# Kernel tuning notes

Hardware: AMD Instinct MI355X
Metric: run time of the kernel (lower is better)

The kernel has to match this reference:

```python
import jax, jax.numpy as jnp
import numpy as np

N_NODES = 100000
N_EDGES = 3200000
IN_DIM = 128
H1, F1 = 8, 8          # layer1: 8 heads x 8 feats -> concat 64
N_CLASSES = 40         # layer2: 1 head -> classes
NEG_SLOPE = 0.2        # GAT LeakyReLU slope


def setup_inputs() -> dict:
    key = jax.random.key(0)
    ks = jax.random.split(key, 8)
    x = jax.random.normal(ks[0], (N_NODES, IN_DIM), dtype=jnp.float32)
    adj = jax.random.randint(ks[1], (2, N_EDGES), 0, N_NODES, dtype=jnp.int64)
    s1 = 1.0 / np.sqrt(IN_DIM)
    s2 = 1.0 / np.sqrt(H1 * F1)
    W1 = jax.random.normal(ks[2], (IN_DIM, H1 * F1), dtype=jnp.float32) * s1
    a1_src = jax.random.normal(ks[3], (H1, F1), dtype=jnp.float32) * s2
    a1_dst = jax.random.normal(ks[4], (H1, F1), dtype=jnp.float32) * s2
    W2 = jax.random.normal(ks[5], (H1 * F1, N_CLASSES), dtype=jnp.float32) * s2
    a2_src = jax.random.normal(ks[6], (1, N_CLASSES), dtype=jnp.float32) * s2
    a2_dst = jax.random.normal(ks[7], (1, N_CLASSES), dtype=jnp.float32) * s2
    return {"input_matrix": x, "adjacency_coo_matrix": adj,
            "W1": W1, "a1_src": a1_src, "a1_dst": a1_dst,
            "W2": W2, "a2_src": a2_src, "a2_dst": a2_dst}


def gat_layer(x, src, dst, W, a_s, a_d, heads, fdim):
    n = x.shape[0]
    h = (x @ W).reshape(n, heads, fdim)                 # [N,H,F]
    e_src = jnp.sum(h * a_s, axis=-1)                   # [N,H]
    e_dst = jnp.sum(h * a_d, axis=-1)                   # [N,H]
    e = jax.nn.leaky_relu(e_src[src] + e_dst[dst], NEG_SLOPE)  # [E,H]
    m = jax.ops.segment_max(e, dst, num_segments=n)     # per-dst softmax max
    p = jnp.exp(e - m[dst])
    s = jax.ops.segment_sum(p, dst, num_segments=n)
    alpha = p / s[dst]                                  # [E,H]
    out = jax.ops.segment_sum(alpha[:, :, None] * h[src], dst, num_segments=n)
    return out                                          # [N,H,F]


def reference(input_matrix, adjacency_coo_matrix, W1, a1_src, a1_dst, W2, a2_src, a2_dst):
    n = input_matrix.shape[0]
    loops = jnp.arange(n, dtype=adjacency_coo_matrix.dtype)
    src = jnp.concatenate([adjacency_coo_matrix[0], loops])
    dst = jnp.concatenate([adjacency_coo_matrix[1], loops])
    x = gat_layer(input_matrix, src, dst, W1, a1_src, a1_dst, H1, F1)
    x = jax.nn.elu(x.reshape(n, H1 * F1))               # concat heads + ELU
    x = gat_layer(x, src, dst, W2, a2_src, a2_dst, 1, N_CLASSES)
    return jax.nn.log_softmax(x.reshape(n, N_CLASSES), axis=1)
```

## Files before the change

### kernel.cpp

```cpp
#include <hip/hip_runtime.h>
#include <hip/hip_fp16.h>
#include <math.h>

#define NN 100000
#define EE 3200000
#define ET (EE + NN)
#define BKW 128
#define NBK ((NN + BKW - 1) / BKW)
#define BCAP 5120
#define EPB 4096
#define NB_P1 ((EE + EPB - 1) / EPB)
#define NB_G 391

typedef float v2f __attribute__((ext_vector_type(2)));
typedef float v4f __attribute__((ext_vector_type(4)));
typedef _Float16 v8h __attribute__((ext_vector_type(8)));

__device__ __forceinline__ float lrelu(float v) { return fmaxf(v, 0.2f * v); }

__device__ __forceinline__ unsigned char to_fp8(float v) {
  return (unsigned char)(__builtin_amdgcn_cvt_pk_fp8_f32(v, v, 0, false) & 0xff);
}


__global__ __launch_bounds__(256) void k_p1g1(
    const int* __restrict__ srcs, const int* __restrict__ dsts,
    int* __restrict__ bcount, int* __restrict__ bbuf,
    const float* __restrict__ x, const float* __restrict__ W1,
    const float* __restrict__ a1d,
    unsigned char* __restrict__ P1, __half* __restrict__ ed1) {
  __shared__ int spk[EPB];
  __shared__ short sbkt[EPB];
  __shared__ int lcnt[NBK];
  __shared__ int excl[NBK];
  __shared__ int gbase[NBK];
  __shared__ int partials[256];
  int tid = threadIdx.x;
  if (blockIdx.x < NB_P1) {
    int e0 = blockIdx.x * EPB;
    int m = min(EPB, EE - e0);
    for (int i = tid; i < NBK; i += 256) lcnt[i] = 0;
    __syncthreads();
    bool valid = (tid * 16) < m;
    int rank[16], bkt[16], pk[16];
    if (valid) {
      const int4* dp = reinterpret_cast<const int4*>(dsts + e0 + tid * 16);
      const int4* sp = reinterpret_cast<const int4*>(srcs + e0 + tid * 16);
      int4 d4[4], s4[4];
#pragma unroll
      for (int i = 0; i < 4; ++i) { d4[i] = dp[i]; s4[i] = sp[i]; }
#pragma unroll
      for (int i = 0; i < 16; ++i) {
        int d = ((const int*)d4)[i];
        int s = ((const int*)s4)[i];
        int b = d >> 7;
        rank[i] = atomicAdd(&lcnt[b], 1);
        bkt[i] = b;
        pk[i] = (s << 7) | (d & 127);
      }
    }
    __syncthreads();
    int b0 = tid * 4;
    int own = 0;
#pragma unroll
    for (int k = 0; k < 4; ++k) {
      int b = b0 + k;
      if (b < NBK) own += lcnt[b];
    }
    partials[tid] = own;
    __syncthreads();
    for (int off = 1; off < 256; off <<= 1) {
      int v = (tid >= off) ? partials[tid - off] : 0;
      __syncthreads();
      partials[tid] += v;
      __syncthreads();
    }
    int run = partials[tid] - own;
#pragma unroll
    for (int k = 0; k < 4; ++k) {
      int b = b0 + k;
      if (b < NBK) {
        excl[b] = run;
        run += lcnt[b];
      }
    }
    for (int i = tid; i < NBK; i += 256) {
      int c = lcnt[i];
      gbase[i] = c ? atomicAdd(&bcount[i], c) : 0;
    }
    __syncthreads();
    if (valid) {
#pragma unroll
      for (int i = 0; i < 16; ++i) {
        int j = excl[bkt[i]] + rank[i];
        spk[j] = pk[i];
        sbkt[j] = (short)bkt[i];
      }
    }
    __syncthreads();
    for (int j = tid; j < m; j += 256) {
      int b = sbkt[j];
      bbuf[(size_t)b * BCAP + gbase[b] + (j - excl[b])] = spk[j];
    }
    return;
  }
  _Float16* Wb = (_Float16*)spk;
  int gbid = blockIdx.x - NB_P1;
  for (int idx = tid; idx < 16 * 64; idx += 256) {
    int f = idx >> 6, l = idx & 63;
    int nt = f >> 2, kk = f & 3;
    int ql = l >> 4, cl = l & 15;
    int col = nt * 16 + cl;
    int k0 = kk * 32 + ql * 8;
    v8h tmp;
#pragma unroll
    for (int j = 0; j < 8; ++j) tmp[j] = (_Float16)W1[(k0 + j) * 64 + col];
    *reinterpret_cast<v8h*>(&Wb[idx * 8]) = tmp;
  }
  __syncthreads();
  int wv = tid >> 6, lane = tid & 63;
  int q = lane >> 4, c = lane & 15;
  v8h bf[16];
#pragma unroll
  for (int f = 0; f < 16; ++f)
    bf[f] = *reinterpret_cast<const v8h*>(&Wb[(f * 64 + lane) * 8]);
  float a1d_l[4];
#pragma unroll
  for (int nt = 0; nt < 4; ++nt) a1d_l[nt] = a1d[nt * 16 + c];
  for (int t = 0; t < 4; ++t) {
    int n0 = gbid * 256 + wv * 64 + t * 16;
    int row = n0 + c;
    row = (row < NN) ? row : (NN - 1);
    v4f acc[4] = {{0.f,0.f,0.f,0.f},{0.f,0.f,0.f,0.f},{0.f,0.f,0.f,0.f},{0.f,0.f,0.f,0.f}};
#pragma unroll
    for (int kk = 0; kk < 4; ++kk) {
      const float* xp = x + (size_t)row * 128 + kk * 32 + q * 8;
      float4 x0 = *reinterpret_cast<const float4*>(xp);
      float4 x1 = *reinterpret_cast<const float4*>(xp + 4);
      v8h af;
      af[0] = (_Float16)x0.x; af[1] = (_Float16)x0.y;
      af[2] = (_Float16)x0.z; af[3] = (_Float16)x0.w;
      af[4] = (_Float16)x1.x; af[5] = (_Float16)x1.y;
      af[6] = (_Float16)x1.z; af[7] = (_Float16)x1.w;
#pragma unroll
      for (int nt = 0; nt < 4; ++nt)
        acc[nt] = __builtin_amdgcn_mfma_f32_16x16x32_f16(af, bf[nt * 4 + kk], acc[nt], 0, 0, 0);
    }
#pragma unroll
    for (int nt = 0; nt < 4; ++nt) {
#pragma unroll
      for (int r = 0; r < 4; ++r) {
        float val = acc[nt][r];
        float vd = val * a1d_l[nt];
        vd += __shfl_xor(vd, 1); vd += __shfl_xor(vd, 2); vd += __shfl_xor(vd, 4);
        int node = n0 + q * 4 + r;
        if (node < NN) {
          P1[((size_t)node << 6) + nt * 16 + c] = to_fp8(val);
          if ((c & 7) == 0) ed1[node * 8 + 2 * nt + (c >> 3)] = __float2half(vd);
        }
      }
    }
  }
}


__global__ __launch_bounds__(256) void k_p2(const int* __restrict__ bcount,
                                            const int* __restrict__ bbuf,
                                            int* __restrict__ offsets,
                                            int* __restrict__ edge_src) {
  __shared__ int cnt[BKW];
  __shared__ int s1[BKW];
  __shared__ int cur[BKW];
  __shared__ int red[256];
  __shared__ int sorted[BCAP + BKW];
  int b = blockIdx.x, tid = threadIdx.x;
  int partial = 0;
  for (int j = tid; j < b; j += 256)
    partial += bcount[j] + min(BKW, NN - (j << 7));
  red[tid] = partial;
  __syncthreads();
  for (int off = 128; off >= 1; off >>= 1) {
    if (tid < off) red[tid] += red[tid + off];
    __syncthreads();
  }
  int base = red[0];
  int d0 = b << 7;
  int width = min(BKW, NN - d0);
  int n = bcount[b];
  const int* buf = bbuf + (size_t)b * BCAP;
  if (tid < BKW) cnt[tid] = (tid < width) ? 1 : 0;
  __syncthreads();
  for (int i = tid; i < n; i += 256) atomicAdd(&cnt[buf[i] & 127], 1);
  __syncthreads();
  if (tid < BKW) s1[tid] = cnt[tid];
  __syncthreads();
  for (int off = 1; off < BKW; off <<= 1) {
    int u = (tid < BKW && tid >= off) ? s1[tid - off] : 0;
    __syncthreads();
    if (tid < BKW) s1[tid] += u;
    __syncthreads();
  }
  if (tid < width) {
    int excl = s1[tid] - cnt[tid];
    offsets[d0 + tid] = base + excl;
    sorted[excl] = d0 + tid;
    cur[tid] = excl + 1;
  }
  if (b == 0 && tid == 0) offsets[NN] = ET;
  __syncthreads();
  for (int i = tid; i < n; i += 256) {
    int p = buf[i];
    int pos = atomicAdd(&cur[p & 127], 1);
    sorted[pos] = p >> 7;
  }
  __syncthreads();
  int m = n + width;
  for (int i = tid; i < m; i += 256)
    edge_src[base + i] = sorted[i];
}


__global__ __launch_bounds__(256) void k_agg1(
    const int* __restrict__ offsets, const int* __restrict__ edge_src,
    const unsigned char* __restrict__ P1, const float* __restrict__ a1s,
    const __half* __restrict__ ed1, __half* __restrict__ x2) {
  int wv = threadIdx.x >> 6, lane = threadIdx.x & 63;
  int g = lane >> 3, p = lane & 7;
  int gbase = lane & 56;
  int dst = blockIdx.x * 32 + wv * 8 + g;
  float edv = __half2float(ed1[dst * 8 + p]);
  float4 as0 = *reinterpret_cast<const float4*>(a1s + p * 8);
  float4 as1 = *reinterpret_cast<const float4*>(a1s + p * 8 + 4);
  int beg = offsets[dst], end = offsets[dst + 1];
  int deg = end - beg;
  int md = deg;
#pragma unroll
  for (int o = 8; o < 64; o <<= 1) md = max(md, __shfl_xor(md, o, 64));
  float l = 0.f;
  float a[8] = {0.f, 0.f, 0.f, 0.f, 0.f, 0.f, 0.f, 0.f};
  for (int t = 0; t < md; t += 8) {
    int idx = t + p;
    int ci = beg + ((idx < deg) ? idx : (deg - 1));
    int mysrc = edge_src[ci];
    int src[8]; uint2 raw[8];
#pragma unroll
    for (int i = 0; i < 8; ++i) src[i] = __shfl(mysrc, gbase | i, 64);
#pragma unroll
    for (int i = 0; i < 8; ++i)
      raw[i] = *reinterpret_cast<const uint2*>(P1 + ((size_t)src[i] << 6) + (p << 3));
#pragma unroll
    for (int i = 0; i < 8; ++i) {
      v2f f01 = __builtin_amdgcn_cvt_pk_f32_fp8(raw[i].x, false);
      v2f f23 = __builtin_amdgcn_cvt_pk_f32_fp8(raw[i].x, true);
      v2f f45 = __builtin_amdgcn_cvt_pk_f32_fp8(raw[i].y, false);
      v2f f67 = __builtin_amdgcn_cvt_pk_f32_fp8(raw[i].y, true);
      float es = f01.x * as0.x + f01.y * as0.y + f23.x * as0.z + f23.y * as0.w
               + f45.x * as1.x + f45.y * as1.y + f67.x * as1.z + f67.y * as1.w;
      float e = lrelu(es + edv);
      float pr = (t + i < deg) ? __expf(e) : 0.f;
      l += pr;
      a[0] += pr * f01.x; a[1] += pr * f01.y;
      a[2] += pr * f23.x; a[3] += pr * f23.y;
      a[4] += pr * f45.x; a[5] += pr * f45.y;
      a[6] += pr * f67.x; a[7] += pr * f67.y;
    }
  }
  float rl = 1.f / l;
  union { __half h[8]; uint4 u; } pk;
#pragma unroll
  for (int i = 0; i < 8; ++i) {
    float v = a[i] * rl;
    v = (v > 0.f) ? v : (__expf(v) - 1.f);
    pk.h[i] = __float2half(v);
  }
  *reinterpret_cast<uint4*>(x2 + ((size_t)dst << 6) + (p << 3)) = pk.u;
}


__global__ __launch_bounds__(256) void k_gemm2(
    const __half* __restrict__ x2, const float* __restrict__ W2,
    const float* __restrict__ a2s, const float* __restrict__ a2d,
    unsigned char* __restrict__ P2, float* __restrict__ ed2) {
  __shared__ _Float16 Wb[6 * 64 * 8];
  int tid = threadIdx.x;
  for (int idx = tid; idx < 6 * 64; idx += 256) {
    int f = idx >> 6, l = idx & 63;
    int nt = f >> 1, kk = f & 1;
    int ql = l >> 4, cl = l & 15;
    int col = nt * 16 + cl;
    int k0 = kk * 32 + ql * 8;
    v8h tmp;
#pragma unroll
    for (int j = 0; j < 8; ++j)
      tmp[j] = (col < 40) ? (_Float16)W2[(k0 + j) * 40 + col] : (_Float16)0.f;
    *reinterpret_cast<v8h*>(&Wb[idx * 8]) = tmp;
  }
  __syncthreads();
  int wv = tid >> 6, lane = tid & 63;
  int q = lane >> 4, c = lane & 15;
  v8h bf[6];
#pragma unroll
  for (int f = 0; f < 6; ++f)
    bf[f] = *reinterpret_cast<const v8h*>(&Wb[(f * 64 + lane) * 8]);
  float a2s_l[3], a2d_l[3];
#pragma unroll
  for (int nt = 0; nt < 3; ++nt) {
    int n = nt * 16 + c;
    a2s_l[nt] = (n < 40) ? a2s[n] : 0.f;
    a2d_l[nt] = (n < 40) ? a2d[n] : 0.f;
  }
  for (int t = 0; t < 4; ++t) {
    int n0 = blockIdx.x * 256 + wv * 64 + t * 16;
    int row = n0 + c;
    row = (row < NN) ? row : (NN - 1);
    v4f acc[3] = {{0.f,0.f,0.f,0.f},{0.f,0.f,0.f,0.f},{0.f,0.f,0.f,0.f}};
#pragma unroll
    for (int kk = 0; kk < 2; ++kk) {
      v8h af = *reinterpret_cast<const v8h*>(x2 + (size_t)row * 64 + kk * 32 + q * 8);
#pragma unroll
      for (int nt = 0; nt < 3; ++nt)
        acc[nt] = __builtin_amdgcn_mfma_f32_16x16x32_f16(af, bf[nt * 2 + kk], acc[nt], 0, 0, 0);
    }
#pragma unroll
    for (int r = 0; r < 4; ++r) {
      float v0 = acc[0][r], v1 = acc[1][r], v2 = acc[2][r];
      float s = v0 * a2s_l[0] + v1 * a2s_l[1] + v2 * a2s_l[2];
      float d = v0 * a2d_l[0] + v1 * a2d_l[1] + v2 * a2d_l[2];
      s += __shfl_xor(s, 1); s += __shfl_xor(s, 2); s += __shfl_xor(s, 4); s += __shfl_xor(s, 8);
      d += __shfl_xor(d, 1); d += __shfl_xor(d, 2); d += __shfl_xor(d, 4); d += __shfl_xor(d, 8);
      int node = n0 + q * 4 + r;
      if (node < NN) {
        unsigned char* rec = P2 + ((size_t)node << 6);
        if (c < 8) rec[32 + c] = to_fp8(v2);
        rec[c]      = to_fp8(v0);
        rec[16 + c] = to_fp8(v1);
        if (c == 0) {
          *reinterpret_cast<__half*>(rec + 40) = __float2half(s);
          ed2[node] = d;
        }
      }
    }
  }
}


__global__ __launch_bounds__(256) void k_agg2(
    const int* __restrict__ offsets, const int* __restrict__ edge_src,
    const unsigned char* __restrict__ P2, const float* __restrict__ ed2,
    float* __restrict__ out) {
  int wv = threadIdx.x >> 6, lane = threadIdx.x & 63;
  int g = lane >> 3, p = lane & 7;
  bool act = p < 5;
  int cp = act ? p : 0;
  int dst = blockIdx.x * 32 + wv * 8 + g;
  float edv = ed2[dst];
  int beg = offsets[dst], end = offsets[dst + 1];
  int deg = end - beg;
  int md = deg;
#pragma unroll
  for (int o = 8; o < 64; o <<= 1) md = max(md, __shfl_xor(md, o, 64));
  int gbase = lane & 56;
  float l = 0.f;
  float a[8] = {0.f, 0.f, 0.f, 0.f, 0.f, 0.f, 0.f, 0.f};
  for (int t = 0; t < md; t += 8) {
    int idx = t + p;
    int ci = beg + ((idx < deg) ? idx : (deg - 1));
    int mysrc = edge_src[ci];
    int src[8]; uint2 raw[8];
#pragma unroll
    for (int i = 0; i < 8; ++i) src[i] = __shfl(mysrc, gbase | i, 64);
    float myes = __half2float(*reinterpret_cast<const __half*>(
        P2 + ((size_t)mysrc << 6) + 40));
    float mye = lrelu(myes + edv);
    float mypr = (t + p < deg) ? __expf(mye) : 0.f;
#pragma unroll
    for (int i = 0; i < 8; ++i)
      raw[i] = *reinterpret_cast<const uint2*>(P2 + ((size_t)src[i] << 6) + (cp << 3));
#pragma unroll
    for (int i = 0; i < 8; ++i) {
      float pr = __shfl(mypr, gbase | i, 64);
      v2f f01 = __builtin_amdgcn_cvt_pk_f32_fp8(raw[i].x, false);
      v2f f23 = __builtin_amdgcn_cvt_pk_f32_fp8(raw[i].x, true);
      v2f f45 = __builtin_amdgcn_cvt_pk_f32_fp8(raw[i].y, false);
      v2f f67 = __builtin_amdgcn_cvt_pk_f32_fp8(raw[i].y, true);
      l += pr;
      a[0] += pr * f01.x; a[1] += pr * f01.y;
      a[2] += pr * f23.x; a[3] += pr * f23.y;
      a[4] += pr * f45.x; a[5] += pr * f45.y;
      a[6] += pr * f67.x; a[7] += pr * f67.y;
    }
  }
  float rl = 1.f / l;
  float v[8];
#pragma unroll
  for (int j = 0; j < 8; ++j) v[j] = a[j] * rl;
  float red = act ? fmaxf(fmaxf(fmaxf(v[0], v[1]), fmaxf(v[2], v[3])),
                          fmaxf(fmaxf(v[4], v[5]), fmaxf(v[6], v[7])))
                  : -INFINITY;
#pragma unroll
  for (int o = 1; o < 8; o <<= 1) red = fmaxf(red, __shfl_xor(red, o, 64));
  float se = 0.f;
  if (act) {
#pragma unroll
    for (int j = 0; j < 8; ++j) se += __expf(v[j] - red);
  }
#pragma unroll
  for (int o = 1; o < 8; o <<= 1) se += __shfl_xor(se, o, 64);
  float ls = red + __logf(se);
  if (act) {
    float* op = out + (size_t)dst * 40 + (p << 3);
    *reinterpret_cast<float4*>(op) =
        make_float4(v[0] - ls, v[1] - ls, v[2] - ls, v[3] - ls);
    *reinterpret_cast<float4*>(op + 4) =
        make_float4(v[4] - ls, v[5] - ls, v[6] - ls, v[7] - ls);
  }
}


extern "C" void kernel_launch(void* const* d_in, const int* in_sizes, int n_in,
                              void* d_out, int out_size, void* d_ws, size_t ws_size,
                              hipStream_t stream) {
  const float* x   = (const float*)d_in[0];
  const int*   adj = (const int*)d_in[1];
  const float* W1  = (const float*)d_in[2];
  const float* a1s = (const float*)d_in[3];
  const float* a1d = (const float*)d_in[4];
  const float* W2  = (const float*)d_in[5];
  const float* a2s = (const float*)d_in[6];
  const float* a2d = (const float*)d_in[7];
  float* out = (float*)d_out;

  const int* srcs = adj;
  const int* dsts = adj + EE;

  char* w = (char*)d_ws;
  size_t off = 0;
  auto alloc = [&](size_t bytes) -> void* {
    void* p = w + off;
    off = (off + bytes + 255) & ~(size_t)255;
    return p;
  };
  int* offsets      = (int*)alloc((size_t)(NN + 1) * 4);
  int* edge_src     = (int*)alloc((size_t)ET * 4);
  int* bcount       = (int*)alloc((size_t)NBK * 4);
  unsigned char* P1 = (unsigned char*)alloc((size_t)NN * 64);
  __half* ed1       = (__half*)alloc((size_t)NN * 8 * 2);
  __half* x2        = (__half*)alloc((size_t)NN * 64 * 2);
  int* bbuf         = (int*)alloc((size_t)NBK * BCAP * 4);
  unsigned char* P2 = P1;
  float* ed2 = (float*)ed1;

  hipMemsetAsync(bcount, 0, (size_t)NBK * 4, stream);
  k_p1g1<<<NB_P1 + NB_G, 256, 0, stream>>>(srcs, dsts, bcount, bbuf,
                                           x, W1, a1d, P1, ed1);
  k_p2<<<NBK, 256, 0, stream>>>(bcount, bbuf, offsets, edge_src);

  k_agg1<<<NN / 32, 256, 0, stream>>>(offsets, edge_src, P1, a1s, ed1, x2);
  k_gemm2<<<NB_G, 256, 0, stream>>>(x2, W2, a2s, a2d, P2, ed2);
  k_agg2<<<NN / 32, 256, 0, stream>>>(offsets, edge_src, P2, ed2, out);
}
```

Before: 284.8 us.

## Restructure edge bucketing into per-block sorted segments with offset table gathered in p2

Phase 1 now handles 16384 edges per block. It counts buckets in a first pass, then re-reads the edges and scatters them into a block-local segment of bbuf ordered by bucket, writing each block's bucket offsets into a table. Phase 2 gathers each bucket's pieces from all phase-1 blocks through that table into shared memory and then sorts them as before. This removes the large shared-memory staging arrays and the scattered global writes into per-bucket slots. In exchange, the edge arrays are read twice, phase-2 reads are serial per thread over small chunks, and the design assumes NB_P1 is at most 256 and each bucket holds at most BCAP edges.

```diff
diff --git a/kernel.cpp b/kernel.cpp
--- a/kernel.cpp
+++ b/kernel.cpp
@@ -8,8 +8,9 @@
 #define BKW 128
 #define NBK ((NN + BKW - 1) / BKW)
 #define BCAP 5120
-#define EPB 4096
+#define EPB 16384
 #define NB_P1 ((EE + EPB - 1) / EPB)
+#define TROW (NBK + 1)
 #define NB_G 391
 
 typedef float v2f __attribute__((ext_vector_type(2)));
@@ -25,39 +26,29 @@
 
 __global__ __launch_bounds__(256) void k_p1g1(
     const int* __restrict__ srcs, const int* __restrict__ dsts,
-    int* __restrict__ bcount, int* __restrict__ bbuf,
+    int* __restrict__ bcount, int* __restrict__ bbuf, int* __restrict__ tbl,
     const float* __restrict__ x, const float* __restrict__ W1,
     const float* __restrict__ a1d,
     unsigned char* __restrict__ P1, __half* __restrict__ ed1) {
-  __shared__ int spk[EPB];
-  __shared__ short sbkt[EPB];
-  __shared__ int lcnt[NBK];
-  __shared__ int excl[NBK];
-  __shared__ int gbase[NBK];
-  __shared__ int partials[256];
+  __shared__ char smem[16 * 64 * 8 * 2];
   int tid = threadIdx.x;
   if (blockIdx.x < NB_P1) {
+    int* lcnt     = (int*)smem;
+    int* excl     = lcnt + NBK;
+    int* cur      = excl + NBK;
+    int* partials = cur + NBK;
     int e0 = blockIdx.x * EPB;
     int m = min(EPB, EE - e0);
     for (int i = tid; i < NBK; i += 256) lcnt[i] = 0;
     __syncthreads();
-    bool valid = (tid * 16) < m;
-    int rank[16], bkt[16], pk[16];
-    if (valid) {
-      const int4* dp = reinterpret_cast<const int4*>(dsts + e0 + tid * 16);
-      const int4* sp = reinterpret_cast<const int4*>(srcs + e0 + tid * 16);
-      int4 d4[4], s4[4];
-#pragma unroll
-      for (int i = 0; i < 4; ++i) { d4[i] = dp[i]; s4[i] = sp[i]; }
-#pragma unroll
-      for (int i = 0; i < 16; ++i) {
-        int d = ((const int*)d4)[i];
-        int s = ((const int*)s4)[i];
-        int b = d >> 7;
-        rank[i] = atomicAdd(&lcnt[b], 1);
-        bkt[i] = b;
-        pk[i] = (s << 7) | (d & 127);
-      }
+    for (int i0 = tid * 16; i0 < m; i0 += 4096) {
+      const int4* dp = reinterpret_cast<const int4*>(dsts + e0 + i0);
+      int4 d4[4];
+#pragma unroll
+      for (int j = 0; j < 4; ++j) d4[j] = dp[j];
+#pragma unroll
+      for (int i = 0; i < 16; ++i)
+        atomicAdd(&lcnt[((const int*)d4)[i] >> 7], 1);
     }
     __syncthreads();
     int b0 = tid * 4;
@@ -81,30 +72,37 @@
       int b = b0 + k;
       if (b < NBK) {
         excl[b] = run;
+        cur[b] = run;
         run += lcnt[b];
       }
     }
+    __syncthreads();
+    int trow = blockIdx.x * TROW;
     for (int i = tid; i < NBK; i += 256) {
+      tbl[trow + i] = excl[i];
       int c = lcnt[i];
-      gbase[i] = c ? atomicAdd(&bcount[i], c) : 0;
-    }
-    __syncthreads();
-    if (valid) {
+      if (c) atomicAdd(&bcount[i], c);
+    }
+    if (tid == 0) tbl[trow + NBK] = m;
+    size_t seg = (size_t)blockIdx.x * EPB;
+    for (int i0 = tid * 16; i0 < m; i0 += 4096) {
+      const int4* dp = reinterpret_cast<const int4*>(dsts + e0 + i0);
+      const int4* sp = reinterpret_cast<const int4*>(srcs + e0 + i0);
+      int4 d4[4], s4[4];
+#pragma unroll
+      for (int j = 0; j < 4; ++j) { d4[j] = dp[j]; s4[j] = sp[j]; }
 #pragma unroll
       for (int i = 0; i < 16; ++i) {
-        int j = excl[bkt[i]] + rank[i];
-        spk[j] = pk[i];
-        sbkt[j] = (short)bkt[i];
+        int d = ((const int*)d4)[i];
+        int s = ((const int*)s4)[i];
+        int b = d >> 7;
+        int pos = atomicAdd(&cur[b], 1);
+        bbuf[seg + pos] = (s << 7) | (d & 127);
       }
     }
-    __syncthreads();
-    for (int j = tid; j < m; j += 256) {
-      int b = sbkt[j];
-      bbuf[(size_t)b * BCAP + gbase[b] + (j - excl[b])] = spk[j];
-    }
     return;
   }
-  _Float16* Wb = (_Float16*)spk;
+  _Float16* Wb = (_Float16*)smem;
   int gbid = blockIdx.x - NB_P1;
   for (int idx = tid; idx < 16 * 64; idx += 256) {
     int f = idx >> 6, l = idx & 63;
@@ -166,8 +164,10 @@
 
 __global__ __launch_bounds__(256) void k_p2(const int* __restrict__ bcount,
                                             const int* __restrict__ bbuf,
+                                            const int* __restrict__ tbl,
                                             int* __restrict__ offsets,
                                             int* __restrict__ edge_src) {
+  __shared__ int stage[BCAP];
   __shared__ int cnt[BKW];
   __shared__ int s1[BKW];
   __shared__ int cur[BKW];
@@ -184,13 +184,32 @@
     __syncthreads();
   }
   int base = red[0];
+  __syncthreads();
+  int myexcl = 0, mycnt = 0;
+  if (tid < NB_P1) {
+    myexcl = tbl[tid * TROW + b];
+    mycnt  = tbl[tid * TROW + b + 1] - myexcl;
+  }
+  red[tid] = mycnt;
+  __syncthreads();
+  for (int off = 1; off < 256; off <<= 1) {
+    int v = (tid >= off) ? red[tid - off] : 0;
+    __syncthreads();
+    red[tid] += v;
+    __syncthreads();
+  }
+  int n = red[255];
+  int dstb = red[tid] - mycnt;
+  if (tid < NB_P1) {
+    const int* sb = bbuf + (size_t)tid * EPB + myexcl;
+    for (int k = 0; k < mycnt; ++k) stage[dstb + k] = sb[k];
+  }
+  __syncthreads();
   int d0 = b << 7;
   int width = min(BKW, NN - d0);
-  int n = bcount[b];
-  const int* buf = bbuf + (size_t)b * BCAP;
   if (tid < BKW) cnt[tid] = (tid < width) ? 1 : 0;
   __syncthreads();
-  for (int i = tid; i < n; i += 256) atomicAdd(&cnt[buf[i] & 127], 1);
+  for (int i = tid; i < n; i += 256) atomicAdd(&cnt[stage[i] & 127], 1);
   __syncthreads();
   if (tid < BKW) s1[tid] = cnt[tid];
   __syncthreads();
@@ -209,7 +228,7 @@
   if (b == 0 && tid == 0) offsets[NN] = ET;
   __syncthreads();
   for (int i = tid; i < n; i += 256) {
-    int p = buf[i];
+    int p = stage[i];
     int pos = atomicAdd(&cur[p & 127], 1);
     sorted[pos] = p >> 7;
   }
@@ -447,13 +466,14 @@
   __half* ed1       = (__half*)alloc((size_t)NN * 8 * 2);
   __half* x2        = (__half*)alloc((size_t)NN * 64 * 2);
   int* bbuf         = (int*)alloc((size_t)NBK * BCAP * 4);
+  int* tbl = bbuf + (size_t)NB_P1 * EPB;
   unsigned char* P2 = P1;
   float* ed2 = (float*)ed1;
 
   hipMemsetAsync(bcount, 0, (size_t)NBK * 4, stream);
-  k_p1g1<<<NB_P1 + NB_G, 256, 0, stream>>>(srcs, dsts, bcount, bbuf,
+  k_p1g1<<<NB_P1 + NB_G, 256, 0, stream>>>(srcs, dsts, bcount, bbuf, tbl,
                                            x, W1, a1d, P1, ed1);
-  k_p2<<<NBK, 256, 0, stream>>>(bcount, bbuf, offsets, edge_src);
+  k_p2<<<NBK, 256, 0, stream>>>(bcount, bbuf, tbl, offsets, edge_src);
 
   k_agg1<<<NN / 32, 256, 0, stream>>>(offsets, edge_src, P1, a1s, ed1, x2);
   k_gemm2<<<NB_G, 256, 0, stream>>>(x2, W2, a2s, a2d, P2, ed2);
```

New measurement: 290.8 us. 1.02x slower.
